# Kernel tuning notes

Hardware: AMD Instinct MI355X
Metric: run time of the kernel (lower is better)

The kernel has to match this reference:

```python
import jax, jax.numpy as jnp
import numpy as np

# ProbSparseAttention (Informer-style), mask_flag=False, factor=10, scale=None,
# output_attention=False, dropout never applied in forward.
# L = 2048 -> U_part = u = 10 * ceil(log(2048)) = 80.
U_TOP = 80


def setup_inputs() -> dict:
    key = jax.random.key(0)
    kq, kk, kv, ki = jax.random.split(key, 4)
    B, L, H, D = 2, 2048, 8, 64
    sample_k = U_TOP
    queries = jax.random.normal(kq, (B, L, H, D), dtype=jnp.float32)
    keys = jax.random.normal(kk, (B, L, H, D), dtype=jnp.float32)
    values = jax.random.normal(kv, (B, L, H, D), dtype=jnp.float32)
    # replaces torch.randint(low=0, high=min(L_Q, L_K), size=(L_Q, sample_k))
    index_sample = jax.random.randint(ki, (L, sample_k), 0, L, dtype=jnp.int32)
    return {"queries": queries, "keys": keys, "values": values,
            "index_sample": index_sample}


def reference(queries, keys, values, index_sample):
    B, L_Q, H, D = queries.shape
    L_K = keys.shape[1]
    u = U_TOP  # n_top queries kept (== sample_k here)

    # [B, L, H, D] -> [B, H, L, D]
    Q = jnp.transpose(queries, (0, 2, 1, 3))
    K = jnp.transpose(keys, (0, 2, 1, 3))
    V = jnpp_transpose = jnp.transpose(values, (0, 2, 1, 3))

    # --- _prob_QK: gather sampled keys per query position ---
    # K_sample[b,h,l,s,:] = K[b,h,index_sample[l,s],:]  -> [B,H,L_Q,sample_k,D]
    K_sample = K[:, :, index_sample, :]
    # Q_K_sample: [B,H,L_Q,sample_k]
    Q_K_sample = jnp.einsum('bhld,bhlsd->bhls', Q, K_sample)
    # sparsity measure M = max - mean(sum/L_K)
    M = Q_K_sample.max(axis=-1) - Q_K_sample.sum(axis=-1) / L_K  # [B,H,L_Q]
    _, M_top = jax.lax.top_k(M, u)  # [B,H,u] indices of top queries

    # Q_reduce: [B,H,u,D]
    Q_reduce = jnp.take_along_axis(Q, M_top[..., None], axis=2)
    # sparse scores against ALL keys: [B,H,u,L_K]
    scale = 1.0 / np.sqrt(D).astype(np.float32)
    scores = jnp.einsum('bhud,bhkd->bhuk', Q_reduce, K) * scale

    # --- initial context (mask_flag=False): mean of V broadcast over u slots ---
    V_mean = V.mean(axis=2)  # [B,H,D]
    context = jnp.broadcast_to(V_mean[:, :, None, :], (B, H, u, D))

    # --- update context at selected slots ---
    attn = jax.nn.softmax(scores, axis=-1)          # [B,H,u,L_K]
    upd = jnp.einsum('bhuk,bhkd->bhud', attn, V)    # [B,H,u,D]
    # original clamps index into [0, L_slot-1] where L_slot = u
    idx = jnp.clip(M_top, 0, u - 1)
    b_idx = jnp.arange(B)[:, None, None]
    h_idx = jnp.arange(H)[None, :, None]
    context = context.at[b_idx, h_idx, idx, :].set(upd)

    # [B,H,u,D] -> [B,u,H,D]
    return jnp.transpose(context, (0, 2, 1, 3))
```

## Files before the change

### kernel.cpp

```cpp
#include <hip/hip_runtime.h>
#include <math.h>

#define LQ 2048
#define NH 8
#define DD 64
#define SK 80
#define UTOP 80
#define NB 2
#define CH 32
#define CK2 64
#define CKS 32

__global__ __launch_bounds__(256) void kA_M(const float* __restrict__ Q,
                                            const float* __restrict__ K,
                                            const int* __restrict__ idxs,
                                            float* __restrict__ M) {
    int x = blockIdx.x;
    int h = x & 7;
    int b = (x >> 3) & 1;
    int l = ((x >> 4) << 2) + (threadIdx.x >> 6);
    int lane = threadIdx.x & 63;
    int g = lane >> 4;
    int t = lane & 15;
    const float4* Qrow = (const float4*)(Q + (((size_t)(b * LQ + l) * NH + h) << 6));
    float4 q4 = Qrow[t];
    float maxv = -INFINITY, sumv = 0.f;
    const int* idxrow = idxs + l * SK;
#pragma unroll
    for (int it = 0; it < SK / 4; ++it) {
        int s = (it << 2) + g;
        int kidx = idxrow[s];
        const float4* Krow = (const float4*)(K + (((size_t)(b * LQ + kidx) * NH + h) << 6));
        float4 k4 = Krow[t];
        float p = q4.x * k4.x + q4.y * k4.y + q4.z * k4.z + q4.w * k4.w;
        p += __shfl_xor(p, 1, 16);
        p += __shfl_xor(p, 2, 16);
        p += __shfl_xor(p, 4, 16);
        p += __shfl_xor(p, 8, 16);
        maxv = fmaxf(maxv, p);
        sumv += p;
    }
    maxv = fmaxf(maxv, __shfl_xor(maxv, 16));
    maxv = fmaxf(maxv, __shfl_xor(maxv, 32));
    sumv += __shfl_xor(sumv, 16);
    sumv += __shfl_xor(sumv, 32);
    if (lane == 0) M[(b * NH + h) * LQ + l] = maxv - sumv * (1.f / 2048.f);
}

__global__ __launch_bounds__(256) void kB_topk(const float* __restrict__ M,
                                               int* __restrict__ Mtop,
                                               int* __restrict__ Winfo) {
    int bh = blockIdx.x;
    int tid = threadIdx.x;
    int lane = tid & 63, w = tid >> 6;
    __shared__ unsigned long long keys[LQ];
    __shared__ int hist[256];
    __shared__ int wavered[4];
    __shared__ int s_need;
    __shared__ unsigned long long s_prefix;
    __shared__ int s_cnt;
    __shared__ unsigned long long s_win;
    const float* Mrow = M + bh * LQ;
#pragma unroll
    for (int i = 0; i < 8; ++i) {
        int e = i * 256 + tid;
        unsigned int bits = __float_as_uint(Mrow[e]);
        bits ^= (unsigned int)(((int)bits >> 31)) | 0x80000000u;
        keys[e] = ((unsigned long long)bits << 16) | (unsigned int)(2047 - e);
    }
    if (tid == 0) { s_need = UTOP; s_prefix = 0ull; s_cnt = 0; s_win = ~0ull; }
    __syncthreads();
#pragma unroll
    for (int pass = 0; pass < 6; ++pass) {
        int shift = 40 - pass * 8;
        int need = s_need;
        unsigned long long pref = s_prefix;
        hist[tid] = 0;
        __syncthreads();
        unsigned long long prefmask = ~((1ull << (shift + 8)) - 1ull);
#pragma unroll
        for (int i = 0; i < 8; ++i) {
            unsigned long long k = keys[i * 256 + tid];
            if ((k & prefmask) == pref)
                atomicAdd(&hist[(int)((k >> shift) & 255)], 1);
        }
        __syncthreads();
        int b = 255 - tid;
        int v = hist[b];
        int x = v;
#pragma unroll
        for (int off = 1; off < 64; off <<= 1) {
            int y = __shfl_up(x, off);
            if (lane >= off) x += y;
        }
        if (lane == 63) wavered[w] = x;
        __syncthreads();
        int add = 0;
        for (int ww = 0; ww < w; ++ww) add += wavered[ww];
        int C = x + add;
        if (C >= need && C - v < need) {
            s_need = need - (C - v);
            s_prefix = pref | ((unsigned long long)b << shift);
        }
        __syncthreads();
    }
    unsigned long long kth = s_prefix;
#pragma unroll
    for (int i = 0; i < 8; ++i) {
        unsigned long long k = keys[i * 256 + tid];
        if (k >= kth) {
            int slot = atomicAdd(&s_cnt, 1);
            int q = 2047 - (int)(k & 0xffffu);
            Mtop[bh * UTOP + slot] = q;
            if (q >= UTOP - 1) atomicMin(&s_win, k);
        }
    }
    __syncthreads();
    if (tid == 0) Winfo[bh] = 2047 - (int)(s_win & 0xffffu);
}

__global__ __launch_bounds__(256) void kC_vsum(const float* __restrict__ V,
                                               float* __restrict__ Vsum) {
    int bh = blockIdx.x & 15;
    int b = bh & 1, h = bh >> 1;
    int lc = blockIdx.x >> 4;
    int d = threadIdx.x & 63;
    int lsub = threadIdx.x >> 6;
    float s = 0.f;
#pragma unroll 4
    for (int i = 0; i < 32; ++i) {
        int l = lc * 128 + lsub + (i << 2);
        s += V[(((size_t)(b * LQ + l) * NH + h) << 6) + d];
    }
    __shared__ float sc[256];
    sc[threadIdx.x] = s;
    __syncthreads();
    if (threadIdx.x < 64) {
        float tot = sc[threadIdx.x] + sc[threadIdx.x + 64] + sc[threadIdx.x + 128] + sc[threadIdx.x + 192];
        atomicAdd(&Vsum[(b * NH + h) * DD + d], tot);
    }
}

__global__ __launch_bounds__(256) void kD_attn(const float* __restrict__ Q,
                                               const float* __restrict__ K,
                                               const float* __restrict__ V,
                                               const int* __restrict__ Mtop,
                                               float* __restrict__ part_m,
                                               float* __restrict__ part_l,
                                               float* __restrict__ part_acc) {
    int code = blockIdx.x & 15;
    int b = code & 1, h = code >> 1;
    int bhl = b * NH + h;
    int c = blockIdx.x >> 4;
    __shared__ int topl[UTOP];
    __shared__ __align__(16) float Qs[UTOP][68];
    __shared__ __align__(16) float Ks[CKS][68];
    __shared__ __align__(16) float Vs[CKS][68];
    __shared__ __align__(16) float Ps[UTOP][36];
    int tid = threadIdx.x;
    if (tid < UTOP) topl[tid] = Mtop[bhl * UTOP + tid];
    __syncthreads();
    for (int f = tid; f < UTOP * 16; f += 256) {
        int u = f >> 4, t4 = f & 15;
        const float4* src = (const float4*)(Q + (((size_t)(b * LQ + topl[u]) * NH + h) << 6));
        *((float4*)&Qs[u][t4 << 2]) = src[t4];
    }
    int i = tid >> 4, j = tid & 15;
    const float scale = 0.125f;
    float4 acc[5];
    float m_run[5], l_run[5];
#pragma unroll
    for (int n = 0; n < 5; ++n) {
        acc[n] = make_float4(0.f, 0.f, 0.f, 0.f);
        m_run[n] = -INFINITY;
        l_run[n] = 0.f;
    }
    for (int sc = 0; sc < 2; ++sc) {
        __syncthreads();
        int kbase = c * CK2 + sc * CKS;
        for (int f = tid; f < CKS * 16; f += 256) {
            int k = f >> 4, t4 = f & 15;
            const float4* srck = (const float4*)(K + (((size_t)(b * LQ + kbase + k) * NH + h) << 6));
            *((float4*)&Ks[k][t4 << 2]) = srck[t4];
            const float4* srcv = (const float4*)(V + (((size_t)(b * LQ + kbase + k) * NH + h) << 6));
            *((float4*)&Vs[k][t4 << 2]) = srcv[t4];
        }
        __syncthreads();
        float s0[5], s1[5];
#pragma unroll
        for (int n = 0; n < 5; ++n) { s0[n] = 0.f; s1[n] = 0.f; }
#pragma unroll
        for (int d4 = 0; d4 < 16; ++d4) {
            float4 ka = *((float4*)&Ks[j][d4 << 2]);
            float4 kb = *((float4*)&Ks[j + 16][d4 << 2]);
#pragma unroll
            for (int n = 0; n < 5; ++n) {
                float4 q4 = *((float4*)&Qs[i * 5 + n][d4 << 2]);
                s0[n] += q4.x * ka.x + q4.y * ka.y + q4.z * ka.z + q4.w * ka.w;
                s1[n] += q4.x * kb.x + q4.y * kb.y + q4.z * kb.z + q4.w * kb.w;
            }
        }
        float m32[5], l32[5];
#pragma unroll
        for (int n = 0; n < 5; ++n) {
            float a = s0[n] * scale, bb = s1[n] * scale;
            float m = fmaxf(a, bb);
#pragma unroll
            for (int off = 1; off < 16; off <<= 1) m = fmaxf(m, __shfl_xor(m, off, 16));
            float p0 = __expf(a - m), p1 = __expf(bb - m);
            float ls = p0 + p1;
#pragma unroll
            for (int off = 1; off < 16; off <<= 1) ls += __shfl_xor(ls, off, 16);
            int u = i * 5 + n;
            Ps[u][j] = p0;
            Ps[u][j + 16] = p1;
            m32[n] = m;
            l32[n] = ls;
        }
        __syncthreads();
        float4 pv[5];
#pragma unroll
        for (int n = 0; n < 5; ++n) pv[n] = make_float4(0.f, 0.f, 0.f, 0.f);
#pragma unroll
        for (int kt = 0; kt < 4; ++kt) {
            float4 pA[5], pB[5];
#pragma unroll
            for (int n = 0; n < 5; ++n) {
                pA[n] = *((float4*)&Ps[i * 5 + n][kt * 8]);
                pB[n] = *((float4*)&Ps[i * 5 + n][kt * 8 + 4]);
            }
#pragma unroll
            for (int kk = 0; kk < 8; ++kk) {
                float4 v4 = *((float4*)&Vs[kt * 8 + kk][j << 2]);
#pragma unroll
                for (int n = 0; n < 5; ++n) {
                    float p = (kk < 4) ? ((float*)&pA[n])[kk] : ((float*)&pB[n])[kk - 4];
                    pv[n].x += p * v4.x; pv[n].y += p * v4.y;
                    pv[n].z += p * v4.z; pv[n].w += p * v4.w;
                }
            }
        }
#pragma unroll
        for (int n = 0; n < 5; ++n) {
            float m_new = fmaxf(m_run[n], m32[n]);
            float fo = __expf(m_run[n] - m_new);
            float fn = __expf(m32[n] - m_new);
            l_run[n] = l_run[n] * fo + l32[n] * fn;
            acc[n].x = acc[n].x * fo + fn * pv[n].x;
            acc[n].y = acc[n].y * fo + fn * pv[n].y;
            acc[n].z = acc[n].z * fo + fn * pv[n].z;
            acc[n].w = acc[n].w * fo + fn * pv[n].w;
            m_run[n] = m_new;
        }
    }
#pragma unroll
    for (int n = 0; n < 5; ++n) {
        int u = i * 5 + n;
        size_t base = ((size_t)(bhl * CH + c) * UTOP + u);
        if (j == 0) {
            part_m[base] = m_run[n];
            part_l[base] = l_run[n];
        }
        *((float4*)&part_acc[base * DD + (j << 2)]) = acc[n];
    }
}

__global__ __launch_bounds__(64) void kE_combine(const float* __restrict__ part_m,
                                                 const float* __restrict__ part_l,
                                                 const float* __restrict__ part_acc,
                                                 float* __restrict__ upd) {
    int bhl = blockIdx.x & 15;
    int u = blockIdx.x >> 4;
    int lane = threadIdx.x;
    float mc = -INFINITY, lc = 0.f;
    if (lane < CH) {
        mc = part_m[(size_t)(bhl * CH + lane) * UTOP + u];
        lc = part_l[(size_t)(bhl * CH + lane) * UTOP + u];
    }
    float m = mc;
#pragma unroll
    for (int off = 1; off < 64; off <<= 1) m = fmaxf(m, __shfl_xor(m, off));
    float alpha = __expf(mc - m);
    float lsum = lc * alpha;
#pragma unroll
    for (int off = 1; off < 64; off <<= 1) lsum += __shfl_xor(lsum, off);
    float accd = 0.f;
    for (int c = 0; c < CH; ++c) {
        float a = __shfl(alpha, c);
        accd += a * part_acc[((size_t)(bhl * CH + c) * UTOP + u) * DD + lane];
    }
    upd[(size_t)(bhl * UTOP + u) * DD + lane] = accd / lsum;
}

__global__ __launch_bounds__(256) void kF_write(const int* __restrict__ Mtop,
                                                const int* __restrict__ Winfo,
                                                const float* __restrict__ upd,
                                                const float* __restrict__ Vsum,
                                                float* __restrict__ out) {
    int bhl = blockIdx.x;
    int b = bhl >> 3, h = bhl & 7;
    __shared__ int winner_row[UTOP];
    int tid = threadIdx.x;
    if (tid < UTOP) winner_row[tid] = -1;
    __syncthreads();
    if (tid < UTOP) {
        int q = Mtop[bhl * UTOP + tid];
        if (q < UTOP - 1) winner_row[q] = tid;
        if (q == Winfo[bhl]) winner_row[UTOP - 1] = tid;
    }
    __syncthreads();
    for (int f = tid; f < UTOP * DD; f += 256) {
        int r = f >> 6, d = f & 63;
        int w = winner_row[r];
        float val = (w >= 0) ? upd[(size_t)(bhl * UTOP + w) * DD + d]
                             : Vsum[bhl * DD + d] * (1.f / 2048.f);
        out[(((size_t)(b * UTOP + r)) * NH + h) * DD + d] = val;
    }
}

extern "C" void kernel_launch(void* const* d_in, const int* in_sizes, int n_in,
                              void* d_out, int out_size, void* d_ws, size_t ws_size,
                              hipStream_t stream) {
    const float* Q = (const float*)d_in[0];
    const float* K = (const float*)d_in[1];
    const float* V = (const float*)d_in[2];
    const int* idxs = (const int*)d_in[3];
    float* out = (float*)d_out;

    char* base = (char*)d_ws;
    float* M        = (float*)(base + 0);
    int*   Mtop     = (int*)  (base + 131072);
    int*   Winfo    = (int*)  (base + 136192);
    float* Vsum     = (float*)(base + 136256);
    float* part_m   = (float*)(base + 140352);
    float* part_l   = (float*)(base + 304192);
    float* part_acc = (float*)(base + 468032);
    float* upd      = (float*)(base + 10953792);

    hipMemsetAsync(Vsum, 0, NB * NH * DD * sizeof(float), stream);

    kA_M   <<<8192, 256, 0, stream>>>(Q, K, idxs, M);
    kB_topk<<<16,   256, 0, stream>>>(M, Mtop, Winfo);
    kC_vsum<<<256,  256, 0, stream>>>(V, Vsum);
    kD_attn<<<16 * CH, 256, 0, stream>>>(Q, K, V, Mtop, part_m, part_l, part_acc);
    kE_combine<<<16 * UTOP, 64, 0, stream>>>(part_m, part_l, part_acc, upd);
    kF_write<<<16, 256, 0, stream>>>(Mtop, Winfo, upd, Vsum, out);
}
```

Measured before the change: 146.6 us.

## Fold V-mean into kA_M, scatter from combine, hoist gathered K loads

The V column sum and the broadcast write of the mean into the output move into 16 extra blocks of the M-scoring kernel. The separate vsum kernel, its memset and atomics, the final write kernel and the upd buffer are all removed. The combine kernel now writes winning rows straight into the output, and blocks that lose the scatter return early. kA_M also issues all 20 gathered K loads before the dot products to raise memory-level parallelism, at the cost of more registers. Correctness depends on kE running after the mean rows are written, which stream ordering provides.

New measurement: 137.0 us. 6.5% less time.

```diff
diff --git a/kernel.cpp b/kernel.cpp
--- a/kernel.cpp
+++ b/kernel.cpp
@@ -13,25 +13,65 @@
 
 __global__ __launch_bounds__(256) void kA_M(const float* __restrict__ Q,
                                             const float* __restrict__ K,
+                                            const float* __restrict__ V,
                                             const int* __restrict__ idxs,
-                                            float* __restrict__ M) {
+                                            float* __restrict__ M,
+                                            float* __restrict__ out) {
+    __shared__ float4 red[16][16];
+    int tid = threadIdx.x;
     int x = blockIdx.x;
+    if (x < 16) {
+        int b = x >> 3, h = x & 7;
+        int d4 = tid & 15, ls = tid >> 4;
+        const float4* V4 = (const float4*)V;
+        float4 s = make_float4(0.f, 0.f, 0.f, 0.f);
+        for (int i = 0; i < 128; ++i) {
+            int l = (i << 4) + ls;
+            float4 v = V4[(((size_t)(b * LQ + l) * NH + h) << 4) + d4];
+            s.x += v.x; s.y += v.y; s.z += v.z; s.w += v.w;
+        }
+        red[ls][d4] = s;
+        __syncthreads();
+        if (ls == 0) {
+            float4 t = red[0][d4];
+            for (int k = 1; k < 16; ++k) {
+                float4 r = red[k][d4];
+                t.x += r.x; t.y += r.y; t.z += r.z; t.w += r.w;
+            }
+            t.x *= (1.f / 2048.f); t.y *= (1.f / 2048.f);
+            t.z *= (1.f / 2048.f); t.w *= (1.f / 2048.f);
+            red[0][d4] = t;
+        }
+        __syncthreads();
+        float4* out4 = (float4*)out;
+        for (int f = tid; f < UTOP * 16; f += 256) {
+            int r = f >> 4, dd = f & 15;
+            out4[(((size_t)(b * UTOP + r) * NH + h) << 4) + dd] = red[0][dd];
+        }
+        return;
+    }
+    x -= 16;
     int h = x & 7;
     int b = (x >> 3) & 1;
-    int l = ((x >> 4) << 2) + (threadIdx.x >> 6);
-    int lane = threadIdx.x & 63;
+    int l = ((x >> 4) << 2) + (tid >> 6);
+    int lane = tid & 63;
     int g = lane >> 4;
     int t = lane & 15;
     const float4* Qrow = (const float4*)(Q + (((size_t)(b * LQ + l) * NH + h) << 6));
     float4 q4 = Qrow[t];
+    const int* idxrow = idxs + l * SK;
+    int kidx[20];
+#pragma unroll
+    for (int it = 0; it < 20; ++it) kidx[it] = idxrow[(it << 2) + g];
+    const float4* K4 = (const float4*)K;
+    float4 kb[20];
+#pragma unroll
+    for (int it = 0; it < 20; ++it)
+        kb[it] = K4[(((size_t)(b * LQ + kidx[it]) * NH + h) << 4) + t];
     float maxv = -INFINITY, sumv = 0.f;
-    const int* idxrow = idxs + l * SK;
-#pragma unroll
-    for (int it = 0; it < SK / 4; ++it) {
-        int s = (it << 2) + g;
-        int kidx = idxrow[s];
-        const float4* Krow = (const float4*)(K + (((size_t)(b * LQ + kidx) * NH + h) << 6));
-        float4 k4 = Krow[t];
+#pragma unroll
+    for (int it = 0; it < 20; ++it) {
+        float4 k4 = kb[it];
         float p = q4.x * k4.x + q4.y * k4.y + q4.z * k4.z + q4.w * k4.w;
         p += __shfl_xor(p, 1, 16);
         p += __shfl_xor(p, 2, 16);
@@ -117,28 +157,6 @@
     }
     __syncthreads();
     if (tid == 0) Winfo[bh] = 2047 - (int)(s_win & 0xffffu);
-}
-
-__global__ __launch_bounds__(256) void kC_vsum(const float* __restrict__ V,
-                                               float* __restrict__ Vsum) {
-    int bh = blockIdx.x & 15;
-    int b = bh & 1, h = bh >> 1;
-    int lc = blockIdx.x >> 4;
-    int d = threadIdx.x & 63;
-    int lsub = threadIdx.x >> 6;
-    float s = 0.f;
-#pragma unroll 4
-    for (int i = 0; i < 32; ++i) {
-        int l = lc * 128 + lsub + (i << 2);
-        s += V[(((size_t)(b * LQ + l) * NH + h) << 6) + d];
-    }
-    __shared__ float sc[256];
-    sc[threadIdx.x] = s;
-    __syncthreads();
-    if (threadIdx.x < 64) {
-        float tot = sc[threadIdx.x] + sc[threadIdx.x + 64] + sc[threadIdx.x + 128] + sc[threadIdx.x + 192];
-        atomicAdd(&Vsum[(b * NH + h) * DD + d], tot);
-    }
 }
 
 __global__ __launch_bounds__(256) void kD_attn(const float* __restrict__ Q,
@@ -268,9 +286,15 @@
 __global__ __launch_bounds__(64) void kE_combine(const float* __restrict__ part_m,
                                                  const float* __restrict__ part_l,
                                                  const float* __restrict__ part_acc,
-                                                 float* __restrict__ upd) {
+                                                 const int* __restrict__ Mtop,
+                                                 const int* __restrict__ Winfo,
+                                                 float* __restrict__ out) {
     int bhl = blockIdx.x & 15;
     int u = blockIdx.x >> 4;
+    int q = Mtop[bhl * UTOP + u];
+    int r;
+    if (q < UTOP - 1) r = q;
+    else { if (q != Winfo[bhl]) return; r = UTOP - 1; }
     int lane = threadIdx.x;
     float mc = -INFINITY, lc = 0.f;
     if (lane < CH) {
@@ -289,33 +313,8 @@
         float a = __shfl(alpha, c);
         accd += a * part_acc[((size_t)(bhl * CH + c) * UTOP + u) * DD + lane];
     }
-    upd[(size_t)(bhl * UTOP + u) * DD + lane] = accd / lsum;
-}
-
-__global__ __launch_bounds__(256) void kF_write(const int* __restrict__ Mtop,
-                                                const int* __restrict__ Winfo,
-                                                const float* __restrict__ upd,
-                                                const float* __restrict__ Vsum,
-                                                float* __restrict__ out) {
-    int bhl = blockIdx.x;
     int b = bhl >> 3, h = bhl & 7;
-    __shared__ int winner_row[UTOP];
-    int tid = threadIdx.x;
-    if (tid < UTOP) winner_row[tid] = -1;
-    __syncthreads();
-    if (tid < UTOP) {
-        int q = Mtop[bhl * UTOP + tid];
-        if (q < UTOP - 1) winner_row[q] = tid;
-        if (q == Winfo[bhl]) winner_row[UTOP - 1] = tid;
-    }
-    __syncthreads();
-    for (int f = tid; f < UTOP * DD; f += 256) {
-        int r = f >> 6, d = f & 63;
-        int w = winner_row[r];
-        float val = (w >= 0) ? upd[(size_t)(bhl * UTOP + w) * DD + d]
-                             : Vsum[bhl * DD + d] * (1.f / 2048.f);
-        out[(((size_t)(b * UTOP + r)) * NH + h) * DD + d] = val;
-    }
+    out[(((size_t)(b * UTOP + r)) * NH + h) * DD + lane] = accd / lsum;
 }
 
 extern "C" void kernel_launch(void* const* d_in, const int* in_sizes, int n_in,
@@ -331,18 +330,12 @@
     float* M        = (float*)(base + 0);
     int*   Mtop     = (int*)  (base + 131072);
     int*   Winfo    = (int*)  (base + 136192);
-    float* Vsum     = (float*)(base + 136256);
-    float* part_m   = (float*)(base + 140352);
-    float* part_l   = (float*)(base + 304192);
-    float* part_acc = (float*)(base + 468032);
-    float* upd      = (float*)(base + 10953792);
-
-    hipMemsetAsync(Vsum, 0, NB * NH * DD * sizeof(float), stream);
-
-    kA_M   <<<8192, 256, 0, stream>>>(Q, K, idxs, M);
+    float* part_m   = (float*)(base + 136256);
+    float* part_l   = (float*)(base + 300096);
+    float* part_acc = (float*)(base + 463936);
+
+    kA_M   <<<8192 + 16, 256, 0, stream>>>(Q, K, V, idxs, M, out);
     kB_topk<<<16,   256, 0, stream>>>(M, Mtop, Winfo);
-    kC_vsum<<<256,  256, 0, stream>>>(V, Vsum);
     kD_attn<<<16 * CH, 256, 0, stream>>>(Q, K, V, Mtop, part_m, part_l, part_acc);
-    kE_combine<<<16 * UTOP, 64, 0, stream>>>(part_m, part_l, part_acc, upd);
-    kF_write<<<16, 256, 0, stream>>>(Mtop, Winfo, upd, Vsum, out);
-}
+    kE_combine<<<16 * UTOP, 64, 0, stream>>>(part_m, part_l, part_acc, Mtop, Winfo, out);
+}
```
